# Kernel tuning notes

Measured on AMD Instinct MI355X. Metric: run time of the kernel, lower is better.

The kernel has to match this reference:

```python
import jax, jax.numpy as jnp
import numpy as np

N = 100000          # nodes
E = 3200000         # edges (avg degree 32)
IN_DIM = 256
HIDDEN = 64
OUT_DIM = 2
K = 10
ALPHA = 0.1
AVG_DEG = 32.0


def setup_inputs() -> dict:
    key = jax.random.key(0)
    ks = jax.random.split(key, 7)
    x = jax.random.normal(ks[0], (N, IN_DIM), dtype=jnp.float32)
    W1 = jax.random.normal(ks[1], (HIDDEN, IN_DIM), dtype=jnp.float32) * (1.0 / np.sqrt(IN_DIM))
    b1 = jnp.zeros((HIDDEN,), dtype=jnp.float32)
    W2 = jax.random.normal(ks[2], (OUT_DIM, HIDDEN), dtype=jnp.float32) * (1.0 / np.sqrt(HIDDEN))
    b2 = jnp.zeros((OUT_DIM,), dtype=jnp.float32)
    edge_rows = jax.random.randint(ks[3], (E,), 0, N, dtype=jnp.int32)
    edge_cols = jax.random.randint(ks[4], (E,), 0, N, dtype=jnp.int32)
    # normalized-adjacency-like values: row sums ~ 0.5 so the K-step power
    # iteration stays stable (mimics D^-1 A normalization)
    edge_vals = jax.random.uniform(ks[5], (E,), dtype=jnp.float32) / AVG_DEG
    return {"x": x, "W1": W1, "b1": b1, "W2": W2, "b2": b2,
            "edge_rows": edge_rows, "edge_cols": edge_cols, "edge_vals": edge_vals}


def reference(x, W1, b1, W2, b2, edge_rows, edge_cols, edge_vals):
    # MLP encoder (dropout is identity at inference)
    h = jax.nn.relu(x @ W1.T + b1)              # [N, HIDDEN]
    Z = h @ W2.T + b2                            # [N, OUT_DIM]

    # APPNP propagation: H <- alpha*Z + (1-alpha) * S @ H, K times
    def step(H, _):
        msg = edge_vals[:, None] * H[edge_cols]  # gather along cols, [E, OUT_DIM]
        SH = jax.ops.segment_sum(msg, edge_rows, num_segments=N)  # scatter-add to rows
        return ALPHA * Z + (1.0 - ALPHA) * SH, None

    H, _ = jax.lax.scan(step, Z, None, length=K)
    return H
```

## Files before the change

kernel.cpp:

```cpp
#include <hip/hip_runtime.h>

#define IN_DIM 256
#define HID 64
#define K_ITERS 10
#define ALPHA 0.1f

constexpr int RPB      = 128;
constexpr int BCAP     = 4992;
constexpr int OVF_CAP  = 8192;
constexpr int MAXBUCK  = 784;
constexpr int CHUNK    = 6272;

typedef __attribute__((ext_vector_type(8))) short short8v;
typedef __attribute__((ext_vector_type(4))) float float4v;

__device__ __forceinline__ unsigned short f32_bf16(float f) {
  unsigned u = __float_as_uint(f);
  u += 0x7FFFu + ((u >> 16) & 1u);
  return (unsigned short)(u >> 16);
}
__device__ __forceinline__ float bf16_f32(unsigned short h) {
  return __uint_as_float((unsigned)h << 16);
}

__global__ __launch_bounds__(256) void w1_frag(
    const float* __restrict__ W1, unsigned short* __restrict__ W1F,
    int* __restrict__ gcnt, int* __restrict__ ovfN, int nbuck)
{
  int idx = blockIdx.x * 256 + threadIdx.x;
  if (blockIdx.x == 0) {
    for (int b = threadIdx.x; b < nbuck; b += 256) gcnt[b] = 0;
    if (threadIdx.x == 0) *ovfN = 0;
  }
  int i  = idx & 7;
  int ln = (idx >> 3) & 63;
  int ht = (idx >> 9) & 3;
  int ks = idx >> 11;
  int hid = ht * 16 + (ln & 15);
  int k   = ks * 32 + (ln >> 4) * 8 + i;
  float v = W1[hid * IN_DIM + k];
  unsigned short hi = f32_bf16(v);
  unsigned short lo = f32_bf16(v - bf16_f32(hi));
  W1F[idx]         = hi;
  W1F[16384 + idx] = lo;
}

__global__ __launch_bounds__(256) void mlp_mfma(
    const float* __restrict__ x, const unsigned short* __restrict__ W1F,
    const float* __restrict__ b1, const float* __restrict__ W2,
    const float* __restrict__ b2, float* __restrict__ Z, int n)
{
  const int tid  = threadIdx.x;
  const int w    = tid >> 6;
  const int lane = tid & 63;
  const int m    = lane & 15;
  const int kg   = lane >> 4;
  const int node = blockIdx.x * 64 + w * 16 + m;
  const bool valid = node < n;
  const float* xrow = x + (size_t)(valid ? node : 0) * IN_DIM;

  const short8v* Bhi = reinterpret_cast<const short8v*>(W1F);
  const short8v* Blo = Bhi + 2048;

  float4v acc[4];
  #pragma unroll
  for (int ht = 0; ht < 4; ++ht) acc[ht] = (float4v){0.f, 0.f, 0.f, 0.f};

  #pragma unroll
  for (int ks = 0; ks < 8; ++ks) {
    const int kb = ks * 32 + kg * 8;
    float4 a0 = *reinterpret_cast<const float4*>(xrow + kb);
    float4 a1 = *reinterpret_cast<const float4*>(xrow + kb + 4);
    float xv[8] = {a0.x, a0.y, a0.z, a0.w, a1.x, a1.y, a1.z, a1.w};
    short8v ahi, alo;
    #pragma unroll
    for (int i = 0; i < 8; ++i) {
      unsigned short h = f32_bf16(xv[i]);
      ahi[i] = (short)h;
      alo[i] = (short)f32_bf16(xv[i] - bf16_f32(h));
    }
    #pragma unroll
    for (int ht = 0; ht < 4; ++ht) {
      int bidx = (ks * 4 + ht) * 64 + lane;
      short8v bh = Bhi[bidx];
      short8v bl = Blo[bidx];
      acc[ht] = __builtin_amdgcn_mfma_f32_16x16x32_bf16(ahi, bh, acc[ht], 0, 0, 0);
      acc[ht] = __builtin_amdgcn_mfma_f32_16x16x32_bf16(alo, bh, acc[ht], 0, 0, 0);
      acc[ht] = __builtin_amdgcn_mfma_f32_16x16x32_bf16(ahi, bl, acc[ht], 0, 0, 0);
    }
  }

  float p0[4] = {0.f, 0.f, 0.f, 0.f}, p1[4] = {0.f, 0.f, 0.f, 0.f};
  #pragma unroll
  for (int ht = 0; ht < 4; ++ht) {
    int hid = ht * 16 + m;
    float w0 = W2[hid], w1v = W2[HID + hid], bb = b1[hid];
    #pragma unroll
    for (int j = 0; j < 4; ++j) {
      float h = fmaxf(acc[ht][j] + bb, 0.f);
      p0[j] = fmaf(h, w0, p0[j]);
      p1[j] = fmaf(h, w1v, p1[j]);
    }
  }
  #pragma unroll
  for (int j = 0; j < 4; ++j) {
    #pragma unroll
    for (int s = 1; s < 16; s <<= 1) {
      p0[j] += __shfl_xor(p0[j], s);
      p1[j] += __shfl_xor(p1[j], s);
    }
  }
  if (m == 0) {
    #pragma unroll
    for (int j = 0; j < 4; ++j) {
      int nd = blockIdx.x * 64 + w * 16 + kg * 4 + j;
      if (nd < n) {
        Z[(size_t)nd * 2 + 0] = p0[j] + b2[0];
        Z[(size_t)nd * 2 + 1] = p1[j] + b2[1];
      }
    }
  }
}

__global__ __launch_bounds__(512) void bucket_build2(
    const int* __restrict__ rows, const int* __restrict__ cols,
    const float* __restrict__ vals, int* __restrict__ gcnt,
    int2* __restrict__ binned, int4* __restrict__ ovf, int* __restrict__ ovfN,
    int e, int nbuck)
{
  __shared__ int2 buf[CHUNK];
  __shared__ unsigned short sb[CHUNK];
  __shared__ int h1[MAXBUCK];
  __shared__ int scn[MAXBUCK];
  __shared__ int lofs[MAXBUCK];
  __shared__ int cur[MAXBUCK];
  __shared__ int gbase[MAXBUCK];

  const int tid = threadIdx.x;
  const int beg = blockIdx.x * CHUNK;
  const int end = min(beg + CHUNK, e);
  const int cnt = end - beg;

  for (int b = tid; b < nbuck; b += 512) h1[b] = 0;
  __syncthreads();

  for (int i = beg + tid; i < end; i += 512)
    atomicAdd(&h1[rows[i] >> 7], 1);
  __syncthreads();

  const int b0 = tid, b1 = tid + 512;
  if (b0 < nbuck) scn[b0] = h1[b0];
  if (b1 < nbuck) scn[b1] = h1[b1];
  __syncthreads();
  for (int off = 1; off < nbuck; off <<= 1) {
    int t0 = 0, t1 = 0;
    if (b0 < nbuck) t0 = scn[b0] + ((b0 >= off) ? scn[b0 - off] : 0);
    if (b1 < nbuck) t1 = scn[b1] + ((b1 >= off) ? scn[b1 - off] : 0);
    __syncthreads();
    if (b0 < nbuck) scn[b0] = t0;
    if (b1 < nbuck) scn[b1] = t1;
    __syncthreads();
  }
  for (int b = tid; b < nbuck; b += 512) {
    int ex = (b == 0) ? 0 : scn[b - 1];
    lofs[b] = ex;
    cur[b]  = ex;
  }
  __syncthreads();

  for (int i = beg + tid; i < end; i += 512) {
    int r = rows[i];
    int b = r >> 7;
    int pos = atomicAdd(&cur[b], 1);
    buf[pos] = make_int2(((r & 127) << 17) | cols[i], __float_as_int(vals[i]));
    sb[pos]  = (unsigned short)b;
  }
  for (int b = tid; b < nbuck; b += 512)
    gbase[b] = h1[b] ? atomicAdd(&gcnt[b], h1[b]) : 0;
  __syncthreads();

  for (int i = tid; i < cnt; i += 512) {
    int b = sb[i];
    int pos = gbase[b] + (i - lofs[b]);
    int2 ed = buf[i];
    if (pos < BCAP) {
      binned[(size_t)b * BCAP + pos] = ed;
    } else {
      int k = atomicAdd(ovfN, 1);
      if (k < OVF_CAP) ovf[k] = make_int4(b, ed.x, ed.y, 0);
    }
  }
}

__global__ __launch_bounds__(512) void bucket_sort(
    const int* __restrict__ gcnt, int2* __restrict__ binned,
    int* __restrict__ rowoff, int nbuck)
{
  __shared__ int2 buf[BCAP];
  __shared__ int hist[RPB];
  __shared__ int offs[RPB];
  __shared__ int cur[RPB];
  const int b = blockIdx.x, tid = threadIdx.x;
  const int cnt = min(gcnt[b], BCAP);
  int2* gp = binned + (size_t)b * BCAP;

  if (tid < RPB) hist[tid] = 0;
  __syncthreads();
  for (int i = tid; i < cnt; i += 512) {
    int2 e = gp[i];
    buf[i] = e;
    atomicAdd(&hist[e.x >> 17], 1);
  }
  __syncthreads();
  if (tid == 0) {
    int run = 0;
    for (int r = 0; r < RPB; ++r) { offs[r] = run; cur[r] = run; run += hist[r]; }
  }
  __syncthreads();
  if (tid < RPB) rowoff[b * RPB + tid] = offs[tid];
  for (int i = tid; i < cnt; i += 512) {
    int2 e = buf[i];
    int pos = atomicAdd(&cur[e.x >> 17], 1);
    gp[pos] = e;
  }
}

__global__ __launch_bounds__(256) void sorted_gather(
    const int* __restrict__ rowoff, const int* __restrict__ gcnt,
    const int2* __restrict__ binned, const float* __restrict__ Z,
    const float* __restrict__ Hin, float* __restrict__ Hout,
    const int4* __restrict__ ovf, const int* __restrict__ ovfN,
    float cB, int n)
{
  int g = blockIdx.x * 256 + threadIdx.x;
  int r = g >> 2, l = g & 3;
  if (r >= n) return;
  int b = r >> 7, rl = r & 127;
  int cntraw = gcnt[b];
  int cnt = min(cntraw, BCAP);
  int beg = rowoff[b * RPB + rl];
  int end = (rl == RPB - 1) ? cnt : rowoff[b * RPB + rl + 1];
  const int2* bp = binned + (size_t)b * BCAP;
  float sx = 0.f, sy = 0.f;

  const int astart = (beg + 1) & ~1;
  if (l == 0 && beg < astart && beg < end) {
    int2 p0 = bp[beg];
    float v = __int_as_float(p0.y);
    float2 h = *reinterpret_cast<const float2*>(&Hin[(size_t)(p0.x & 0x1FFFF) * 2]);
    sx = fmaf(v, h.x, sx); sy = fmaf(v, h.y, sy);
  }
  int npair = (end > astart) ? ((end - astart) >> 1) : 0;
  if (l == 1 && end > astart && ((end - astart) & 1)) {
    int2 p0 = bp[end - 1];
    float v = __int_as_float(p0.y);
    float2 h = *reinterpret_cast<const float2*>(&Hin[(size_t)(p0.x & 0x1FFFF) * 2]);
    sx = fmaf(v, h.x, sx); sy = fmaf(v, h.y, sy);
  }
  const int4* bp4 = reinterpret_cast<const int4*>(bp) + (astart >> 1);

  int4 eb[8];
  #pragma unroll
  for (int c = 0; c < 8; ++c) {
    int k = l + 4 * c;
    if (k < npair) eb[c] = bp4[k];
  }
  #pragma unroll
  for (int c = 0; c < 8; ++c) {
    int k = l + 4 * c;
    if (k < npair) {
      int4 p = eb[c];
      float vA = __int_as_float(p.y), vB = __int_as_float(p.w);
      float2 hA = *reinterpret_cast<const float2*>(&Hin[(size_t)(p.x & 0x1FFFF) * 2]);
      float2 hB = *reinterpret_cast<const float2*>(&Hin[(size_t)(p.z & 0x1FFFF) * 2]);
      sx = fmaf(vA, hA.x, fmaf(vB, hB.x, sx));
      sy = fmaf(vA, hA.y, fmaf(vB, hB.y, sy));
    }
  }
  for (int k = l + 32; k < npair; k += 4) {
    int4 p = bp4[k];
    float vA = __int_as_float(p.y), vB = __int_as_float(p.w);
    float2 hA = *reinterpret_cast<const float2*>(&Hin[(size_t)(p.x & 0x1FFFF) * 2]);
    float2 hB = *reinterpret_cast<const float2*>(&Hin[(size_t)(p.z & 0x1FFFF) * 2]);
    sx = fmaf(vA, hA.x, fmaf(vB, hB.x, sx));
    sy = fmaf(vA, hA.y, fmaf(vB, hB.y, sy));
  }

  if (cntraw > BCAP) {
    int mo = min(*ovfN, OVF_CAP);
    for (int j = l; j < mo; j += 4) {
      int4 o = ovf[j];
      if (o.x == b && (o.y >> 17) == rl) {
        int col = o.y & 0x1FFFF;
        float v = __int_as_float(o.z);
        float2 h = *reinterpret_cast<const float2*>(&Hin[(size_t)col * 2]);
        sx += v * h.x; sy += v * h.y;
      }
    }
  }
  sx += __shfl_xor(sx, 1); sy += __shfl_xor(sy, 1);
  sx += __shfl_xor(sx, 2); sy += __shfl_xor(sy, 2);
  if (l == 0) {
    float2 z = *reinterpret_cast<const float2*>(&Z[(size_t)r * 2]);
    reinterpret_cast<float2*>(Hout)[r] =
        make_float2(ALPHA * z.x + cB * sx, ALPHA * z.y + cB * sy);
  }
}

extern "C" void kernel_launch(void* const* d_in, const int* in_sizes, int n_in,
                              void* d_out, int out_size, void* d_ws, size_t ws_size,
                              hipStream_t stream) {
  const float* x     = (const float*)d_in[0];
  const float* W1    = (const float*)d_in[1];
  const float* b1    = (const float*)d_in[2];
  const float* W2    = (const float*)d_in[3];
  const float* b2    = (const float*)d_in[4];
  const int*   erows = (const int*)d_in[5];
  const int*   ecols = (const int*)d_in[6];
  const float* evals = (const float*)d_in[7];
  float* out = (float*)d_out;

  const int n = in_sizes[0] / IN_DIM;
  const int e = in_sizes[5];
  const int nbuck = (n + RPB - 1) / RPB;

  char* ws = (char*)d_ws;
  int2*  binned = (int2*)ws;            ws += (size_t)nbuck * BCAP * sizeof(int2);
  int4*  ovf    = (int4*)ws;            ws += (size_t)OVF_CAP * sizeof(int4);
  float* Z      = (float*)ws;           ws += (size_t)n * 2 * sizeof(float);
  float* Ha     = (float*)ws;           ws += (size_t)n * 2 * sizeof(float);
  float* Hb     = (float*)ws;           ws += (size_t)n * 2 * sizeof(float);
  unsigned short* W1F = (unsigned short*)ws;  ws += 2 * 16384 * sizeof(unsigned short);
  int*   rowoff = (int*)ws;             ws += (size_t)nbuck * RPB * sizeof(int);
  int*   gcnt   = (int*)ws;             ws += (size_t)nbuck * sizeof(int);
  int*   ovfN   = (int*)ws;             ws += 4 * sizeof(int);

  w1_frag<<<64, 256, 0, stream>>>(W1, W1F, gcnt, ovfN, nbuck);

  const int grid_b = (e + CHUNK - 1) / CHUNK;
  bucket_build2<<<grid_b, 512, 0, stream>>>(erows, ecols, evals, gcnt,
                                            binned, ovf, ovfN, e, nbuck);
  bucket_sort<<<nbuck, 512, 0, stream>>>(gcnt, binned, rowoff, nbuck);

  mlp_mfma<<<(n + 63) / 64, 256, 0, stream>>>(x, W1F, b1, W2, b2, Z, n);

  const float cB = 1.f - ALPHA;
  const int grid_g = (4 * n + 255) / 256;
  const float* hin = Z;
  for (int t = 0; t < K_ITERS; ++t) {
    float* hout = (t == K_ITERS - 1) ? out : ((t & 1) ? Hb : Ha);
    sorted_gather<<<grid_g, 256, 0, stream>>>(rowoff, gcnt, binned, Z, hin, hout,
                                              ovf, ovfN, cB, n);
    hin = hout;
  }
}
```

Before: 297.2 us.

## Fuse edge bucket build and MLP encoder into one heterogeneous-block launch

Merges the bucket_build2 and mlp_mfma kernels into a single launch. The first gb blocks bin edges and the remaining blocks compute the MLP with two 64-node groups per 512-thread block. This lets the memory-bound edge binning overlap with the MFMA encoder and removes one launch boundary. The cost is that MLP blocks now carry the build kernel's large shared-memory footprint, which lowers their occupancy, and every block pays for the union of register usage.

```diff
diff --git a/kernel.cpp b/kernel.cpp
--- a/kernel.cpp
+++ b/kernel.cpp
@@ -45,88 +45,14 @@
   W1F[16384 + idx] = lo;
 }
 
-__global__ __launch_bounds__(256) void mlp_mfma(
+__global__ __launch_bounds__(512) void fused_build_mlp(
+    const int* __restrict__ rows, const int* __restrict__ cols,
+    const float* __restrict__ vals, int* __restrict__ gcnt,
+    int2* __restrict__ binned, int4* __restrict__ ovf, int* __restrict__ ovfN,
+    int e, int nbuck, int gb,
     const float* __restrict__ x, const unsigned short* __restrict__ W1F,
     const float* __restrict__ b1, const float* __restrict__ W2,
     const float* __restrict__ b2, float* __restrict__ Z, int n)
-{
-  const int tid  = threadIdx.x;
-  const int w    = tid >> 6;
-  const int lane = tid & 63;
-  const int m    = lane & 15;
-  const int kg   = lane >> 4;
-  const int node = blockIdx.x * 64 + w * 16 + m;
-  const bool valid = node < n;
-  const float* xrow = x + (size_t)(valid ? node : 0) * IN_DIM;
-
-  const short8v* Bhi = reinterpret_cast<const short8v*>(W1F);
-  const short8v* Blo = Bhi + 2048;
-
-  float4v acc[4];
-  #pragma unroll
-  for (int ht = 0; ht < 4; ++ht) acc[ht] = (float4v){0.f, 0.f, 0.f, 0.f};
-
-  #pragma unroll
-  for (int ks = 0; ks < 8; ++ks) {
-    const int kb = ks * 32 + kg * 8;
-    float4 a0 = *reinterpret_cast<const float4*>(xrow + kb);
-    float4 a1 = *reinterpret_cast<const float4*>(xrow + kb + 4);
-    float xv[8] = {a0.x, a0.y, a0.z, a0.w, a1.x, a1.y, a1.z, a1.w};
-    short8v ahi, alo;
-    #pragma unroll
-    for (int i = 0; i < 8; ++i) {
-      unsigned short h = f32_bf16(xv[i]);
-      ahi[i] = (short)h;
-      alo[i] = (short)f32_bf16(xv[i] - bf16_f32(h));
-    }
-    #pragma unroll
-    for (int ht = 0; ht < 4; ++ht) {
-      int bidx = (ks * 4 + ht) * 64 + lane;
-      short8v bh = Bhi[bidx];
-      short8v bl = Blo[bidx];
-      acc[ht] = __builtin_amdgcn_mfma_f32_16x16x32_bf16(ahi, bh, acc[ht], 0, 0, 0);
-      acc[ht] = __builtin_amdgcn_mfma_f32_16x16x32_bf16(alo, bh, acc[ht], 0, 0, 0);
-      acc[ht] = __builtin_amdgcn_mfma_f32_16x16x32_bf16(ahi, bl, acc[ht], 0, 0, 0);
-    }
-  }
-
-  float p0[4] = {0.f, 0.f, 0.f, 0.f}, p1[4] = {0.f, 0.f, 0.f, 0.f};
-  #pragma unroll
-  for (int ht = 0; ht < 4; ++ht) {
-    int hid = ht * 16 + m;
-    float w0 = W2[hid], w1v = W2[HID + hid], bb = b1[hid];
-    #pragma unroll
-    for (int j = 0; j < 4; ++j) {
-      float h = fmaxf(acc[ht][j] + bb, 0.f);
-      p0[j] = fmaf(h, w0, p0[j]);
-      p1[j] = fmaf(h, w1v, p1[j]);
-    }
-  }
-  #pragma unroll
-  for (int j = 0; j < 4; ++j) {
-    #pragma unroll
-    for (int s = 1; s < 16; s <<= 1) {
-      p0[j] += __shfl_xor(p0[j], s);
-      p1[j] += __shfl_xor(p1[j], s);
-    }
-  }
-  if (m == 0) {
-    #pragma unroll
-    for (int j = 0; j < 4; ++j) {
-      int nd = blockIdx.x * 64 + w * 16 + kg * 4 + j;
-      if (nd < n) {
-        Z[(size_t)nd * 2 + 0] = p0[j] + b2[0];
-        Z[(size_t)nd * 2 + 1] = p1[j] + b2[1];
-      }
-    }
-  }
-}
-
-__global__ __launch_bounds__(512) void bucket_build2(
-    const int* __restrict__ rows, const int* __restrict__ cols,
-    const float* __restrict__ vals, int* __restrict__ gcnt,
-    int2* __restrict__ binned, int4* __restrict__ ovf, int* __restrict__ ovfN,
-    int e, int nbuck)
 {
   __shared__ int2 buf[CHUNK];
   __shared__ unsigned short sb[CHUNK];
@@ -137,57 +63,134 @@
   __shared__ int gbase[MAXBUCK];
 
   const int tid = threadIdx.x;
-  const int beg = blockIdx.x * CHUNK;
-  const int end = min(beg + CHUNK, e);
-  const int cnt = end - beg;
-
-  for (int b = tid; b < nbuck; b += 512) h1[b] = 0;
-  __syncthreads();
-
-  for (int i = beg + tid; i < end; i += 512)
-    atomicAdd(&h1[rows[i] >> 7], 1);
-  __syncthreads();
-
-  const int b0 = tid, b1 = tid + 512;
-  if (b0 < nbuck) scn[b0] = h1[b0];
-  if (b1 < nbuck) scn[b1] = h1[b1];
-  __syncthreads();
-  for (int off = 1; off < nbuck; off <<= 1) {
-    int t0 = 0, t1 = 0;
-    if (b0 < nbuck) t0 = scn[b0] + ((b0 >= off) ? scn[b0 - off] : 0);
-    if (b1 < nbuck) t1 = scn[b1] + ((b1 >= off) ? scn[b1 - off] : 0);
-    __syncthreads();
-    if (b0 < nbuck) scn[b0] = t0;
-    if (b1 < nbuck) scn[b1] = t1;
-    __syncthreads();
-  }
-  for (int b = tid; b < nbuck; b += 512) {
-    int ex = (b == 0) ? 0 : scn[b - 1];
-    lofs[b] = ex;
-    cur[b]  = ex;
-  }
-  __syncthreads();
-
-  for (int i = beg + tid; i < end; i += 512) {
-    int r = rows[i];
-    int b = r >> 7;
-    int pos = atomicAdd(&cur[b], 1);
-    buf[pos] = make_int2(((r & 127) << 17) | cols[i], __float_as_int(vals[i]));
-    sb[pos]  = (unsigned short)b;
-  }
-  for (int b = tid; b < nbuck; b += 512)
-    gbase[b] = h1[b] ? atomicAdd(&gcnt[b], h1[b]) : 0;
-  __syncthreads();
-
-  for (int i = tid; i < cnt; i += 512) {
-    int b = sb[i];
-    int pos = gbase[b] + (i - lofs[b]);
-    int2 ed = buf[i];
-    if (pos < BCAP) {
-      binned[(size_t)b * BCAP + pos] = ed;
-    } else {
-      int k = atomicAdd(ovfN, 1);
-      if (k < OVF_CAP) ovf[k] = make_int4(b, ed.x, ed.y, 0);
+
+  if (blockIdx.x < (unsigned)gb) {
+    const int beg = blockIdx.x * CHUNK;
+    const int end = min(beg + CHUNK, e);
+    const int cnt = end - beg;
+
+    for (int b = tid; b < nbuck; b += 512) h1[b] = 0;
+    __syncthreads();
+
+    for (int i = beg + tid; i < end; i += 512)
+      atomicAdd(&h1[rows[i] >> 7], 1);
+    __syncthreads();
+
+    const int b0 = tid, b1i = tid + 512;
+    if (b0 < nbuck) scn[b0] = h1[b0];
+    if (b1i < nbuck) scn[b1i] = h1[b1i];
+    __syncthreads();
+    for (int off = 1; off < nbuck; off <<= 1) {
+      int t0 = 0, t1 = 0;
+      if (b0 < nbuck) t0 = scn[b0] + ((b0 >= off) ? scn[b0 - off] : 0);
+      if (b1i < nbuck) t1 = scn[b1i] + ((b1i >= off) ? scn[b1i - off] : 0);
+      __syncthreads();
+      if (b0 < nbuck) scn[b0] = t0;
+      if (b1i < nbuck) scn[b1i] = t1;
+      __syncthreads();
+    }
+    for (int b = tid; b < nbuck; b += 512) {
+      int ex = (b == 0) ? 0 : scn[b - 1];
+      lofs[b] = ex;
+      cur[b]  = ex;
+    }
+    __syncthreads();
+
+    for (int i = beg + tid; i < end; i += 512) {
+      int r = rows[i];
+      int b = r >> 7;
+      int pos = atomicAdd(&cur[b], 1);
+      buf[pos] = make_int2(((r & 127) << 17) | cols[i], __float_as_int(vals[i]));
+      sb[pos]  = (unsigned short)b;
+    }
+    for (int b = tid; b < nbuck; b += 512)
+      gbase[b] = h1[b] ? atomicAdd(&gcnt[b], h1[b]) : 0;
+    __syncthreads();
+
+    for (int i = tid; i < cnt; i += 512) {
+      int b = sb[i];
+      int pos = gbase[b] + (i - lofs[b]);
+      int2 ed = buf[i];
+      if (pos < BCAP) {
+        binned[(size_t)b * BCAP + pos] = ed;
+      } else {
+        int k = atomicAdd(ovfN, 1);
+        if (k < OVF_CAP) ovf[k] = make_int4(b, ed.x, ed.y, 0);
+      }
+    }
+  } else {
+    const int bi   = blockIdx.x - gb;
+    const int grp  = tid >> 8;
+    const int t8   = tid & 255;
+    const int w    = t8 >> 6;
+    const int lane = tid & 63;
+    const int m    = lane & 15;
+    const int kg   = lane >> 4;
+    const int nb   = bi * 128 + grp * 64;
+    const int node = nb + w * 16 + m;
+    const bool valid = node < n;
+    const float* xrow = x + (size_t)(valid ? node : 0) * IN_DIM;
+
+    const short8v* Bhi = reinterpret_cast<const short8v*>(W1F);
+    const short8v* Blo = Bhi + 2048;
+
+    float4v acc[4];
+    #pragma unroll
+    for (int ht = 0; ht < 4; ++ht) acc[ht] = (float4v){0.f, 0.f, 0.f, 0.f};
+
+    #pragma unroll
+    for (int ks = 0; ks < 8; ++ks) {
+      const int kb = ks * 32 + kg * 8;
+      float4 a0 = *reinterpret_cast<const float4*>(xrow + kb);
+      float4 a1 = *reinterpret_cast<const float4*>(xrow + kb + 4);
+      float xv[8] = {a0.x, a0.y, a0.z, a0.w, a1.x, a1.y, a1.z, a1.w};
+      short8v ahi, alo;
+      #pragma unroll
+      for (int i = 0; i < 8; ++i) {
+        unsigned short h = f32_bf16(xv[i]);
+        ahi[i] = (short)h;
+        alo[i] = (short)f32_bf16(xv[i] - bf16_f32(h));
+      }
+      #pragma unroll
+      for (int ht = 0; ht < 4; ++ht) {
+        int bidx = (ks * 4 + ht) * 64 + lane;
+        short8v bh = Bhi[bidx];
+        short8v bl = Blo[bidx];
+        acc[ht] = __builtin_amdgcn_mfma_f32_16x16x32_bf16(ahi, bh, acc[ht], 0, 0, 0);
+        acc[ht] = __builtin_amdgcn_mfma_f32_16x16x32_bf16(alo, bh, acc[ht], 0, 0, 0);
+        acc[ht] = __builtin_amdgcn_mfma_f32_16x16x32_bf16(ahi, bl, acc[ht], 0, 0, 0);
+      }
+    }
+
+    float p0[4] = {0.f, 0.f, 0.f, 0.f}, p1[4] = {0.f, 0.f, 0.f, 0.f};
+    #pragma unroll
+    for (int ht = 0; ht < 4; ++ht) {
+      int hid = ht * 16 + m;
+      float w0 = W2[hid], w1v = W2[HID + hid], bb = b1[hid];
+      #pragma unroll
+      for (int j = 0; j < 4; ++j) {
+        float h = fmaxf(acc[ht][j] + bb, 0.f);
+        p0[j] = fmaf(h, w0, p0[j]);
+        p1[j] = fmaf(h, w1v, p1[j]);
+      }
+    }
+    #pragma unroll
+    for (int j = 0; j < 4; ++j) {
+      #pragma unroll
+      for (int s = 1; s < 16; s <<= 1) {
+        p0[j] += __shfl_xor(p0[j], s);
+        p1[j] += __shfl_xor(p1[j], s);
+      }
+    }
+    if (m == 0) {
+      #pragma unroll
+      for (int j = 0; j < 4; ++j) {
+        int nd = nb + w * 16 + kg * 4 + j;
+        if (nd < n) {
+          Z[(size_t)nd * 2 + 0] = p0[j] + b2[0];
+          Z[(size_t)nd * 2 + 1] = p1[j] + b2[1];
+        }
+      }
     }
   }
 }
@@ -337,12 +340,13 @@
 
   w1_frag<<<64, 256, 0, stream>>>(W1, W1F, gcnt, ovfN, nbuck);
 
-  const int grid_b = (e + CHUNK - 1) / CHUNK;
-  bucket_build2<<<grid_b, 512, 0, stream>>>(erows, ecols, evals, gcnt,
-                                            binned, ovf, ovfN, e, nbuck);
+  const int gb = (e + CHUNK - 1) / CHUNK;
+  const int gm = (n + 127) / 128;
+  fused_build_mlp<<<gb + gm, 512, 0, stream>>>(erows, ecols, evals, gcnt,
+                                               binned, ovf, ovfN, e, nbuck, gb,
+                                               x, W1F, b1, W2, b2, Z, n);
+
   bucket_sort<<<nbuck, 512, 0, stream>>>(gcnt, binned, rowoff, nbuck);
-
-  mlp_mfma<<<(n + 63) / 64, 256, 0, stream>>>(x, W1F, b1, W2, b2, Z, n);
 
   const float cB = 1.f - ALPHA;
   const int grid_g = (4 * n + 255) / 256;
```

Result: no change. 299.6 us (+0.8%).
